# Kernel tuning notes

Hardware: AMD Instinct MI355X
Metric: run time of the kernel (lower is better)

The kernel has to match this reference:

```python
import jax, jax.numpy as jnp
import numpy as np

N_NODES = 50000
IN_CH = 128
DIM = 32
HEADS = 8
OUT_CH = 2
NEG_SLOPE = 0.2


def _glorot(key, shape):
    fan_in = shape[0]
    return jax.random.normal(key, shape, dtype=jnp.float32) / jnp.sqrt(jnp.float32(fan_in))


def gatv2_conv(x, Wl, bl, Wr, br, att, bias, src, dst, n_nodes, heads, out_c, concat):
    """PyG GATv2Conv (eval mode, add_self_loops already applied to src/dst)."""
    xl = (x @ Wl + bl).reshape(n_nodes, heads, out_c)  # [N,H,C] source transform
    xr = (x @ Wr + br).reshape(n_nodes, heads, out_c)  # [N,H,C] target transform
    # per-edge GATv2 score: a^T LeakyReLU(xl[j] + xr[i])
    e = jax.nn.leaky_relu(xl[src] + xr[dst], NEG_SLOPE)          # [E,H,C]
    score = jnp.einsum('ehc,hc->eh', e, att)                      # [E,H]
    # segment softmax over incoming edges of each target node
    smax = jax.ops.segment_max(score, dst, num_segments=n_nodes)  # [N,H]
    ex = jnp.exp(score - smax[dst])
    denom = jax.ops.segment_sum(ex, dst, num_segments=n_nodes)
    alpha = ex / (denom[dst] + 1e-16)                             # [E,H]
    out = jax.ops.segment_sum(alpha[:, :, None] * xl[src], dst, num_segments=n_nodes)  # [N,H,C]
    if concat:
        out = out.reshape(n_nodes, heads * out_c)
    else:
        out = out.mean(axis=1)
    return out + bias


def setup_inputs() -> dict:
    key = jax.random.key(0)
    ks = jax.random.split(key, 20)
    x = jax.random.normal(ks[0], (N_NODES, IN_CH), dtype=jnp.float32)
    edge_index = jax.random.randint(ks[1], (2, 400000), 0, N_NODES, dtype=jnp.int32)
    H, C = HEADS, DIM
    hid = H * C  # 256
    params = {
        'Wl1': _glorot(ks[2], (IN_CH, hid)), 'bl1': jnp.zeros((hid,), jnp.float32),
        'Wr1': _glorot(ks[3], (IN_CH, hid)), 'br1': jnp.zeros((hid,), jnp.float32),
        'att1': _glorot(ks[4], (H, C)), 'b1': jnp.zeros((hid,), jnp.float32),
        'Wl3': _glorot(ks[5], (hid, hid)), 'bl3': jnp.zeros((hid,), jnp.float32),
        'Wr3': _glorot(ks[6], (hid, hid)), 'br3': jnp.zeros((hid,), jnp.float32),
        'att3': _glorot(ks[7], (H, C)), 'b3': jnp.zeros((hid,), jnp.float32),
        'Wl2': _glorot(ks[8], (hid, OUT_CH)), 'bl2': jnp.zeros((OUT_CH,), jnp.float32),
        'Wr2': _glorot(ks[9], (hid, OUT_CH)), 'br2': jnp.zeros((OUT_CH,), jnp.float32),
        'att2': _glorot(ks[10], (1, OUT_CH)), 'b2': jnp.zeros((OUT_CH,), jnp.float32),
    }
    return {'x': x, 'edge_index': edge_index, **params}


def reference(x, edge_index, Wl1, bl1, Wr1, br1, att1, b1,
              Wl3, bl3, Wr3, br3, att3, b3,
              Wl2, bl2, Wr2, br2, att2, b2):
    n = x.shape[0]
    loop = jnp.arange(n, dtype=edge_index.dtype)
    src = jnp.concatenate([edge_index[0], loop])  # PyG add_self_loops
    dst = jnp.concatenate([edge_index[1], loop])
    # dropout layers are no-ops in eval mode
    h = jax.nn.elu(gatv2_conv(x, Wl1, bl1, Wr1, br1, att1, b1, src, dst, n, HEADS, DIM, True))
    h = jax.nn.elu(gatv2_conv(h, Wl3, bl3, Wr3, br3, att3, b3, src, dst, n, HEADS, DIM, True))
    h = gatv2_conv(h, Wl2, bl2, Wr2, br2, att2, b2, src, dst, n, 1, OUT_CH, False)
    return jax.nn.log_softmax(h, axis=-1)
```

## Files before the change

### kernel.cpp

```cpp
#include <hip/hip_runtime.h>
#include <cstdint>
#include <cstddef>


typedef __attribute__((ext_vector_type(8))) _Float16 v8h;
typedef __attribute__((ext_vector_type(2))) _Float16 h2;
typedef __attribute__((ext_vector_type(2))) __fp16 h2r;
typedef __attribute__((ext_vector_type(4))) float v4f;

__device__ __forceinline__ float lrelu(float v) { return fmaxf(v, 0.2f * v); }
__device__ __forceinline__ float elu1(float v)  { return v > 0.f ? v : expm1f(v); }

__device__ __forceinline__ unsigned short f2h(float f) {
  _Float16 h = (_Float16)f;
  return __builtin_bit_cast(unsigned short, h);
}
__device__ __forceinline__ float h2f(unsigned short s) {
  return (float)__builtin_bit_cast(_Float16, s);
}

__device__ __forceinline__ h2 cvt_pk(float a, float b) {
  h2r t = __builtin_amdgcn_cvt_pkrtz(a, b);
  return __builtin_bit_cast(h2, t);
}
__device__ __forceinline__ h2 pk2(float a) { return cvt_pk(a, a); }

__device__ __forceinline__ h2 lrelu_pk(h2 v) {
  unsigned int u = __builtin_bit_cast(unsigned int, v) & 0x7FFF7FFFu;
  h2 av = __builtin_bit_cast(h2, u);
  h2 c6 = {(_Float16)0.6f, (_Float16)0.6f};
  h2 c4 = {(_Float16)0.4f, (_Float16)0.4f};
  return v * c6 + av * c4;
}

__device__ __forceinline__ float dot2(h2 a, h2 b, float c) {
#if __has_builtin(__builtin_amdgcn_fdot2)
  return __builtin_amdgcn_fdot2(__builtin_bit_cast(h2r, a),
                                __builtin_bit_cast(h2r, b), c, false);
#else
  return fmaf((float)a[0], (float)b[0], fmaf((float)a[1], (float)b[1], c));
#endif
}

__device__ __forceinline__ void gl_lds16(const void* g, void* l) {
  __builtin_amdgcn_global_load_lds(
      (const __attribute__((address_space(1))) unsigned int*)g,
      (__attribute__((address_space(3))) unsigned int*)l, 16, 0, 0);
}


__global__ void k_count(const int* __restrict__ dst, int* __restrict__ deg, int E) {
  int e = blockIdx.x * blockDim.x + threadIdx.x;
  if (e < E) atomicAdd(&deg[dst[e]], 1);
}

__global__ __launch_bounds__(256) void k_bsum(const int* __restrict__ deg, int n,
                                              int* __restrict__ bsum) {
  __shared__ int red[256];
  int t = threadIdx.x, bid = blockIdx.x;
  int i0 = bid * 1024 + t * 4;
  int s = 0;
  if (i0 + 3 < n) {
    int4 v = *(const int4*)&deg[i0];
    s = v.x + v.y + v.z + v.w;
  } else {
#pragma unroll
    for (int j = 0; j < 4; ++j)
      if (i0 + j < n) s += deg[i0 + j];
  }
  red[t] = s;
  __syncthreads();
  for (int off = 128; off > 0; off >>= 1) {
    if (t < off) red[t] += red[t + off];
    __syncthreads();
  }
  if (t == 0) bsum[bid] = red[0];
}

__global__ __launch_bounds__(256) void k_offsets(const int* __restrict__ deg,
                                                 const int* __restrict__ bsum,
                                                 int nb, int n,
                                                 int* __restrict__ offs,
                                                 int* __restrict__ cursor) {
  __shared__ int sc[256];
  int t = threadIdx.x, bid = blockIdx.x;
  int base = 0;
  for (int b = 0; b < bid; ++b) base += bsum[b];
  int i0 = bid * 1024 + t * 4;
  int v0 = 0, v1 = 0, v2 = 0, v3 = 0;
  if (i0 + 3 < n) {
    int4 v = *(const int4*)&deg[i0];
    v0 = v.x; v1 = v.y; v2 = v.z; v3 = v.w;
  } else {
    if (i0 < n)     v0 = deg[i0];
    if (i0 + 1 < n) v1 = deg[i0 + 1];
    if (i0 + 2 < n) v2 = deg[i0 + 2];
    if (i0 + 3 < n) v3 = deg[i0 + 3];
  }
  int s = v0 + v1 + v2 + v3;
  sc[t] = s;
  __syncthreads();
  for (int off = 1; off < 256; off <<= 1) {
    int x = (t >= off) ? sc[t - off] : 0;
    __syncthreads();
    sc[t] += x;
    __syncthreads();
  }
  int run = base + sc[t] - s;
  int o0 = run, o1 = run + v0, o2 = o1 + v1, o3 = o2 + v2;
  if (i0 + 3 < n) {
    *(int4*)&offs[i0] = make_int4(o0, o1, o2, o3);
    *(int4*)&cursor[i0] = make_int4(o0, o1, o2, o3);
  } else {
    if (i0 < n)     { offs[i0] = o0;     cursor[i0] = o0; }
    if (i0 + 1 < n) { offs[i0 + 1] = o1; cursor[i0 + 1] = o1; }
    if (i0 + 2 < n) { offs[i0 + 2] = o2; cursor[i0 + 2] = o2; }
    if (i0 + 3 < n) { offs[i0 + 3] = o3; cursor[i0 + 3] = o3; }
  }
  if (bid == nb - 1 && t == 255) offs[n] = base + sc[255];
}

__global__ void k_scatter(const int* __restrict__ src, const int* __restrict__ dst,
                          int* __restrict__ cursor, int* __restrict__ csr_src, int E) {
  int e = blockIdx.x * blockDim.x + threadIdx.x;
  if (e < E) {
    int pos = atomicAdd(&cursor[dst[e]], 1);
    csr_src[pos] = src[e];
  }
}


__global__ void k_split(const float* __restrict__ Wl, const float* __restrict__ Wr,
                        int K, int logK, unsigned short* __restrict__ Bt) {
  int idx = blockIdx.x * blockDim.x + threadIdx.x;
  if (idx >= 512 * K) return;
  int n = idx >> logK;
  int k = idx & (K - 1);
  float w = (n < 256) ? Wl[(size_t)k * 256 + n] : Wr[(size_t)k * 256 + (n - 256)];
  Bt[idx] = f2h(w);
}


__global__ void k_quantA(const float* __restrict__ X, int Nreal, int total4,
                         unsigned short* __restrict__ Hh) {
  int idx = blockIdx.x * blockDim.x + threadIdx.x;
  if (idx >= total4) return;
  int row = idx >> 5;
  ushort4 uh;
  if (row < Nreal) {
    float4 v = *(const float4*)&X[(size_t)idx * 4];
    uh.x = f2h(v.x); uh.y = f2h(v.y); uh.z = f2h(v.z); uh.w = f2h(v.w);
  } else {
    uh = make_ushort4(0, 0, 0, 0);
  }
  *(ushort4*)&Hh[(size_t)idx * 4] = uh;
}


__global__ __launch_bounds__(256) void k_gemm_mfma(
    const unsigned short* __restrict__ A_g,
    int Nreal, int K,
    const unsigned short* __restrict__ Bt,
    const float* __restrict__ bl, const float* __restrict__ br,
    unsigned short* __restrict__ xl_h, unsigned short* __restrict__ xr_h) {
  __shared__ __align__(16) short Ah[2][64 * 32];
  __shared__ __align__(16) short Bh[2][256 * 32];

  const int tid = threadIdx.x;
  const int lane = tid & 63;
  const int wid = tid >> 6;
  const int l15 = lane & 15, g = lane >> 4;
  const int bm = blockIdx.x * 64;
  const int half = blockIdx.y;
  const int bn = half * 256;

  v4f acc[4][4];
#pragma unroll
  for (int m = 0; m < 4; ++m)
#pragma unroll
    for (int n = 0; n < 4; ++n) acc[m][n] = (v4f)(0.f);

  const int arow = tid >> 2, aslot = tid & 3;
  const int aoct = aslot ^ ((arow >> 1) & 3);
  const unsigned gaBase = (unsigned)(bm + arow) * K + aoct * 8;

  auto STAGE = [&](int buf, int k0) {
    gl_lds16(A_g + (gaBase + k0), &Ah[buf][wid * 512]);
#pragma unroll
    for (int it = 0; it < 4; ++it) {
      int task = it * 256 + tid;
      int col = task >> 2, slot = task & 3;
      int oct = slot ^ ((col >> 1) & 3);
      unsigned gb = (unsigned)(bn + col) * K + k0 + oct * 8;
      gl_lds16(Bt + gb, &Bh[buf][it * 2048 + wid * 512]);
    }
  };

  const int nt = K >> 5;
  STAGE(0, 0);
  for (int t = 0; t < nt; ++t) {
    const int cur = t & 1;
    if (t + 1 < nt) {
      STAGE(cur ^ 1, (t + 1) << 5);
      asm volatile("s_waitcnt vmcnt(5)" ::: "memory");
    } else {
      asm volatile("s_waitcnt vmcnt(0)" ::: "memory");
    }
    __builtin_amdgcn_sched_barrier(0);
    __builtin_amdgcn_s_barrier();

    v8h a_h[4], b_h[4];
#pragma unroll
    for (int m = 0; m < 4; ++m) {
      int r = m * 16 + l15;
      int s = g ^ ((r >> 1) & 3);
      a_h[m] = *(const v8h*)&Ah[cur][r * 32 + s * 8];
    }
#pragma unroll
    for (int n = 0; n < 4; ++n) {
      int c = wid * 64 + n * 16 + l15;
      int s = g ^ ((c >> 1) & 3);
      b_h[n] = *(const v8h*)&Bh[cur][c * 32 + s * 8];
    }
#pragma unroll
    for (int m = 0; m < 4; ++m)
#pragma unroll
      for (int n = 0; n < 4; ++n)
        acc[m][n] = __builtin_amdgcn_mfma_f32_16x16x32_f16(a_h[m], b_h[n], acc[m][n], 0, 0, 0);
    __builtin_amdgcn_s_barrier();
  }

  float* scr = (float*)&Bh[0][0] + wid * 320;
  const int erow = lane >> 2, ecq = lane & 3;
  unsigned short* outp = half ? xr_h : xl_h;
  const float* bias = half ? br : bl;
#pragma unroll
  for (int m = 0; m < 4; ++m) {
#pragma unroll
    for (int n = 0; n < 4; ++n) {
#pragma unroll
      for (int r = 0; r < 4; ++r) scr[(g * 4 + r) * 20 + l15] = acc[m][n][r];
      float4 v = *(const float4*)&scr[erow * 20 + ecq * 4];
      int row = bm + m * 16 + erow;
      if (row < Nreal) {
        int col = wid * 64 + n * 16 + ecq * 4;
        float4 bv = *(const float4*)&bias[col];
        ushort4 u;
        u.x = f2h(v.x + bv.x); u.y = f2h(v.y + bv.y);
        u.z = f2h(v.z + bv.z); u.w = f2h(v.w + bv.w);
        *(ushort4*)&outp[(size_t)row * 256 + col] = u;
      }
    }
  }
}


__global__ __launch_bounds__(256) void k_edge(
    const unsigned short* __restrict__ xl_h,
    const unsigned short* __restrict__ xr_h,
    const int* __restrict__ offs, const int* __restrict__ csr_src,
    const float* __restrict__ att,
    const float* __restrict__ bias,
    unsigned short* __restrict__ hout,
    int n) {
  int lane = threadIdx.x & 63;
  int node = blockIdx.x * (blockDim.x >> 6) + (threadIdx.x >> 6);
  if (node >= n) return;

  const unsigned lb = (unsigned)(lane << 2);
  float4 attf = *(const float4*)&att[lb];
  h2 atta = cvt_pk(attf.x, attf.y);
  h2 attb = cvt_pk(attf.z, attf.w);
  const unsigned noff = ((unsigned)node << 8) + lb;
  uint2 urx = *(const uint2*)(xr_h + noff);
  h2 xra = __builtin_bit_cast(h2, urx.x), xrb = __builtin_bit_cast(h2, urx.y);

  uint2 us = *(const uint2*)(xl_h + noff);
  h2 acca = __builtin_bit_cast(h2, us.x), accb = __builtin_bit_cast(h2, us.y);
  float p = dot2(lrelu_pk(acca + xra), atta, 0.f);
  p = dot2(lrelu_pk(accb + xrb), attb, p);
  p += __shfl_xor(p, 1);
  p += __shfl_xor(p, 2);
  p += __shfl_xor(p, 4);
  float m = p, d = 1.f;

  int e0 = offs[node], e1 = offs[node + 1];
  int e = e0;
  for (; e + 1 < e1; e += 2) {
    int j1 = csr_src[e], j2 = csr_src[e + 1];
    uint2 u1 = *(const uint2*)(xl_h + (((unsigned)j1 << 8) + lb));
    uint2 u2 = *(const uint2*)(xl_h + (((unsigned)j2 << 8) + lb));
    h2 x1a = __builtin_bit_cast(h2, u1.x), x1b = __builtin_bit_cast(h2, u1.y);
    h2 x2a = __builtin_bit_cast(h2, u2.x), x2b = __builtin_bit_cast(h2, u2.y);
    float p1 = dot2(lrelu_pk(x1a + xra), atta, 0.f);
    p1 = dot2(lrelu_pk(x1b + xrb), attb, p1);
    float p2 = dot2(lrelu_pk(x2a + xra), atta, 0.f);
    p2 = dot2(lrelu_pk(x2b + xrb), attb, p2);
    p1 += __shfl_xor(p1, 1); p2 += __shfl_xor(p2, 1);
    p1 += __shfl_xor(p1, 2); p2 += __shfl_xor(p2, 2);
    p1 += __shfl_xor(p1, 4); p2 += __shfl_xor(p2, 4);
    float m12 = fmaxf(p1, p2);
    float w1 = __expf(p1 - m12), w2 = __expf(p2 - m12);
    float d12 = w1 + w2;
    h2 w1p = pk2(w1), w2p = pk2(w2);
    h2 ca = x1a * w1p + x2a * w2p;
    h2 cb = x1b * w1p + x2b * w2p;
    float mN = fmaxf(m, m12);
    float r  = __expf(m - mN);
    float r2 = __expf(m12 - mN);
    d = fmaf(d, r, d12 * r2);
    h2 rp = pk2(r), r2p = pk2(r2);
    acca = acca * rp + ca * r2p;
    accb = accb * rp + cb * r2p;
    m = mN;
  }
  if (e < e1) {
    int j = csr_src[e];
    uint2 u = *(const uint2*)(xl_h + (((unsigned)j << 8) + lb));
    h2 xa = __builtin_bit_cast(h2, u.x), xb = __builtin_bit_cast(h2, u.y);
    float p1 = dot2(lrelu_pk(xa + xra), atta, 0.f);
    p1 = dot2(lrelu_pk(xb + xrb), attb, p1);
    p1 += __shfl_xor(p1, 1);
    p1 += __shfl_xor(p1, 2);
    p1 += __shfl_xor(p1, 4);
    float mN = fmaxf(m, p1);
    float r = __expf(m - mN), w1 = __expf(p1 - mN);
    d = fmaf(d, r, w1);
    h2 rp = pk2(r), w1p = pk2(w1);
    acca = acca * rp + xa * w1p;
    accb = accb * rp + xb * w1p;
  }

  float inv = 1.f / (d + 1e-16f);
  float4 b4 = *(const float4*)&bias[lb];
  float o0 = elu1(fmaf((float)acca[0], inv, b4.x));
  float o1 = elu1(fmaf((float)acca[1], inv, b4.y));
  float o2 = elu1(fmaf((float)accb[0], inv, b4.z));
  float o3 = elu1(fmaf((float)accb[1], inv, b4.w));
  ushort4 uo;
  uo.x = f2h(o0); uo.y = f2h(o1); uo.z = f2h(o2); uo.w = f2h(o3);
  *(ushort4*)(hout + noff) = uo;
}


__global__ __launch_bounds__(256) void k_lin3(
    const unsigned short* __restrict__ hq,
    const float* __restrict__ Wl, const float* __restrict__ bl,
    const float* __restrict__ Wr, const float* __restrict__ br,
    float* __restrict__ xlr3,
    int n) {
  int lane = threadIdx.x & 63;
  int node = blockIdx.x * (blockDim.x >> 6) + (threadIdx.x >> 6);
  if (node >= n) return;
  ushort4 uh = *(const ushort4*)(hq + (((unsigned)node << 8) + (lane << 2)));
  float hv[4] = {h2f(uh.x), h2f(uh.y), h2f(uh.z), h2f(uh.w)};
  float al0 = 0.f, al1 = 0.f, ar0 = 0.f, ar1 = 0.f;
#pragma unroll
  for (int j = 0; j < 4; ++j) {
    int k = lane * 4 + j;
    al0 = fmaf(hv[j], Wl[k * 2 + 0], al0);
    al1 = fmaf(hv[j], Wl[k * 2 + 1], al1);
    ar0 = fmaf(hv[j], Wr[k * 2 + 0], ar0);
    ar1 = fmaf(hv[j], Wr[k * 2 + 1], ar1);
  }
#pragma unroll
  for (int s = 1; s < 64; s <<= 1) {
    al0 += __shfl_xor(al0, s);
    al1 += __shfl_xor(al1, s);
    ar0 += __shfl_xor(ar0, s);
    ar1 += __shfl_xor(ar1, s);
  }
  if (lane == 0) {
    float4 o = make_float4(al0 + bl[0], al1 + bl[1], ar0 + br[0], ar1 + br[1]);
    *(float4*)&xlr3[(size_t)node * 4] = o;
  }
}


__global__ void k_edge3(const float* __restrict__ xlr3,
                        const int* __restrict__ offs, const int* __restrict__ csr_src,
                        const float* __restrict__ att,
                        const float* __restrict__ b,
                        float* __restrict__ out, int n) {
  int i = blockIdx.x * blockDim.x + threadIdx.x;
  if (i >= n) return;
  float a0 = att[0], a1 = att[1];
  float xr0 = xlr3[(size_t)i * 4 + 2], xr1 = xlr3[(size_t)i * 4 + 3];
  float sl0 = xlr3[(size_t)i * 4 + 0], sl1 = xlr3[(size_t)i * 4 + 1];
  float m = lrelu(sl0 + xr0) * a0 + lrelu(sl1 + xr1) * a1;
  float d = 1.f, ac0 = sl0, ac1 = sl1;
  int e0 = offs[i], e1 = offs[i + 1];
  for (int e = e0; e < e1; ++e) {
    int j = csr_src[e];
    float xl0 = xlr3[(size_t)j * 4 + 0], xl1 = xlr3[(size_t)j * 4 + 1];
    float p = lrelu(xl0 + xr0) * a0 + lrelu(xl1 + xr1) * a1;
    float mN = fmaxf(m, p);
    float r = __expf(m - mN), w = __expf(p - mN);
    d = fmaf(d, r, w);
    ac0 = fmaf(ac0, r, w * xl0);
    ac1 = fmaf(ac1, r, w * xl1);
    m = mN;
  }
  float inv = 1.f / (d + 1e-16f);
  float o0 = fmaf(ac0, inv, b[0]);
  float o1 = fmaf(ac1, inv, b[1]);
  float mx = fmaxf(o0, o1);
  float lse = mx + logf(expf(o0 - mx) + expf(o1 - mx));
  out[(size_t)i * 2 + 0] = o0 - lse;
  out[(size_t)i * 2 + 1] = o1 - lse;
}


static inline size_t align_up(size_t v, size_t a) { return (v + a - 1) & ~(a - 1); }

extern "C" void kernel_launch(void* const* d_in, const int* in_sizes, int n_in,
                              void* d_out, int out_size, void* d_ws, size_t ws_size,
                              hipStream_t stream) {
  const float* x    = (const float*)d_in[0];
  const int*   ei   = (const int*)d_in[1];
  const float* Wl1  = (const float*)d_in[2];
  const float* bl1  = (const float*)d_in[3];
  const float* Wr1  = (const float*)d_in[4];
  const float* br1  = (const float*)d_in[5];
  const float* att1 = (const float*)d_in[6];
  const float* b1   = (const float*)d_in[7];
  const float* Wl3  = (const float*)d_in[8];
  const float* bl3  = (const float*)d_in[9];
  const float* Wr3  = (const float*)d_in[10];
  const float* br3  = (const float*)d_in[11];
  const float* att3 = (const float*)d_in[12];
  const float* b3   = (const float*)d_in[13];
  const float* Wl2  = (const float*)d_in[14];
  const float* bl2  = (const float*)d_in[15];
  const float* Wr2  = (const float*)d_in[16];
  const float* br2  = (const float*)d_in[17];
  const float* att2 = (const float*)d_in[18];
  const float* b2   = (const float*)d_in[19];

  const int N = in_sizes[0] / 128;
  const int E = in_sizes[1] / 2;
  const int Npad = ((N + 63) / 64) * 64;
  const int* srcp = ei;
  const int* dstp = ei + E;

  char* w = (char*)d_ws;
  size_t off = 0;
  int* deg     = (int*)(w + off); off = align_up(off + (size_t)N * 4, 256);
  int* offs    = (int*)(w + off); off = align_up(off + (size_t)(N + 1) * 4, 256);
  int* cursor  = (int*)(w + off); off = align_up(off + (size_t)N * 4, 256);
  int* csr_src = (int*)(w + off); off = align_up(off + (size_t)E * 4, 256);
  int* bsum    = (int*)(w + off); off = align_up(off + (size_t)256 * 4, 256);
  unsigned short* x_h  = (unsigned short*)(w + off); off = align_up(off + (size_t)Npad * 128 * 2, 256);
  unsigned short* h_h  = (unsigned short*)(w + off); off = align_up(off + (size_t)Npad * 256 * 2, 256);
  unsigned short* xlh  = (unsigned short*)(w + off); off = align_up(off + (size_t)N * 256 * 2, 256);
  unsigned short* xrh  = (unsigned short*)(w + off); off = align_up(off + (size_t)N * 256 * 2, 256);
  float* xlr3  = (float*)(w + off); off = align_up(off + (size_t)N * 4 * 4, 256);
  unsigned short* Bt1 = (unsigned short*)(w + off); off = align_up(off + (size_t)512 * 128 * 2, 256);
  unsigned short* Bt2 = (unsigned short*)(w + off); off = align_up(off + (size_t)512 * 256 * 2, 256);
  (void)ws_size;

  const int nb = (N + 1023) / 1024;

  hipMemsetAsync(deg, 0, (size_t)N * 4, stream);
  k_count<<<(E + 255) / 256, 256, 0, stream>>>(dstp, deg, E);
  k_bsum<<<nb, 256, 0, stream>>>(deg, N, bsum);
  k_offsets<<<nb, 256, 0, stream>>>(deg, bsum, nb, N, offs, cursor);
  k_scatter<<<(E + 255) / 256, 256, 0, stream>>>(srcp, dstp, cursor, csr_src, E);

  k_split<<<(512 * 128 + 255) / 256, 256, 0, stream>>>(Wl1, Wr1, 128, 7, Bt1);
  k_split<<<(512 * 256 + 255) / 256, 256, 0, stream>>>(Wl3, Wr3, 256, 8, Bt2);
  {
    int total4 = Npad * 128 / 4;
    k_quantA<<<(total4 + 255) / 256, 256, 0, stream>>>(x, N, total4, x_h);
  }
  hipMemsetAsync(h_h + (size_t)N * 256, 0, (size_t)(Npad - N) * 256 * 2, stream);

  dim3 ggrid(Npad / 64, 2);
  int nodeBlocks = (N + 3) / 4;

  k_gemm_mfma<<<ggrid, 256, 0, stream>>>(x_h, N, 128, Bt1, bl1, br1, xlh, xrh);
  k_edge<<<nodeBlocks, 256, 0, stream>>>(xlh, xrh, offs, csr_src, att1, b1, h_h, N);

  k_gemm_mfma<<<ggrid, 256, 0, stream>>>(h_h, N, 256, Bt2, bl3, br3, xlh, xrh);
  k_edge<<<nodeBlocks, 256, 0, stream>>>(xlh, xrh, offs, csr_src, att3, b3, h_h, N);

  k_lin3<<<nodeBlocks, 256, 0, stream>>>(h_h, Wl2, bl2, Wr2, br2, xlr3, N);
  k_edge3<<<(N + 255) / 256, 256, 0, stream>>>(xlr3, offs, csr_src, att2, b2,
                                               (float*)d_out, N);
}
```

Measured before the change: 240.6 us.

## Process each node with 32 lanes and 16-byte gathers in GATv2 edge kernel

The edge aggregation kernel now assigns 32 lanes per target node instead of 64. Each lane handles 8 fp16 channels through 16-byte loads, so a block covers 8 nodes. Each head's score reduction becomes a 4-lane sum done with DPP quad permutes rather than three shuffle-xor steps. This is meant to cut the number of load instructions and the cross-lane reduction overhead per gathered edge row, at the cost of more registers per lane. The launch grids are adjusted so the per-node block count for k_lin3 stays unchanged.

```diff
diff --git a/kernel.cpp b/kernel.cpp
--- a/kernel.cpp
+++ b/kernel.cpp
@@ -40,6 +40,14 @@
 #else
   return fmaf((float)a[0], (float)b[0], fmaf((float)a[1], (float)b[1], c));
 #endif
+}
+
+__device__ __forceinline__ float quad_sum(float p) {
+  int t1 = __builtin_amdgcn_update_dpp(0, __float_as_int(p), 0xB1, 0xF, 0xF, true);
+  p += __int_as_float(t1);
+  int t2 = __builtin_amdgcn_update_dpp(0, __float_as_int(p), 0x4E, 0xF, 0xF, true);
+  p += __int_as_float(t2);
+  return p;
 }
 
 __device__ __forceinline__ void gl_lds16(const void* g, void* l) {
@@ -263,83 +271,97 @@
     const float* __restrict__ bias,
     unsigned short* __restrict__ hout,
     int n) {
-  int lane = threadIdx.x & 63;
-  int node = blockIdx.x * (blockDim.x >> 6) + (threadIdx.x >> 6);
+  int lane = threadIdx.x & 31;
+  int node = blockIdx.x * (blockDim.x >> 5) + (threadIdx.x >> 5);
   if (node >= n) return;
 
-  const unsigned lb = (unsigned)(lane << 2);
-  float4 attf = *(const float4*)&att[lb];
-  h2 atta = cvt_pk(attf.x, attf.y);
-  h2 attb = cvt_pk(attf.z, attf.w);
-  const unsigned noff = ((unsigned)node << 8) + lb;
-  uint2 urx = *(const uint2*)(xr_h + noff);
-  h2 xra = __builtin_bit_cast(h2, urx.x), xrb = __builtin_bit_cast(h2, urx.y);
-
-  uint2 us = *(const uint2*)(xl_h + noff);
-  h2 acca = __builtin_bit_cast(h2, us.x), accb = __builtin_bit_cast(h2, us.y);
-  float p = dot2(lrelu_pk(acca + xra), atta, 0.f);
-  p = dot2(lrelu_pk(accb + xrb), attb, p);
-  p += __shfl_xor(p, 1);
-  p += __shfl_xor(p, 2);
-  p += __shfl_xor(p, 4);
-  float m = p, d = 1.f;
+  const unsigned cb = ((unsigned)(lane >> 2) << 5) + ((unsigned)(lane & 3) << 3);
+  float4 af0 = *(const float4*)&att[cb];
+  float4 af1 = *(const float4*)&att[cb + 4];
+  h2 att0 = cvt_pk(af0.x, af0.y), att1 = cvt_pk(af0.z, af0.w);
+  h2 att2 = cvt_pk(af1.x, af1.y), att3 = cvt_pk(af1.z, af1.w);
+  const unsigned noff = ((unsigned)node << 8) + cb;
+  uint4 urx = *(const uint4*)(xr_h + noff);
+  h2 xr0 = __builtin_bit_cast(h2, urx.x), xr1 = __builtin_bit_cast(h2, urx.y);
+  h2 xr2 = __builtin_bit_cast(h2, urx.z), xr3 = __builtin_bit_cast(h2, urx.w);
+  const unsigned short* xlb = xl_h + cb;
+
+  auto score = [&](h2 a, h2 b, h2 c, h2 dd) -> float {
+    float p = dot2(lrelu_pk(a + xr0), att0, 0.f);
+    p = dot2(lrelu_pk(b + xr1), att1, p);
+    p = dot2(lrelu_pk(c + xr2), att2, p);
+    p = dot2(lrelu_pk(dd + xr3), att3, p);
+    return quad_sum(p);
+  };
+
+  uint4 us = *(const uint4*)(xl_h + noff);
+  h2 a0 = __builtin_bit_cast(h2, us.x), a1 = __builtin_bit_cast(h2, us.y);
+  h2 a2 = __builtin_bit_cast(h2, us.z), a3 = __builtin_bit_cast(h2, us.w);
+  float m = score(a0, a1, a2, a3), d = 1.f;
 
   int e0 = offs[node], e1 = offs[node + 1];
   int e = e0;
   for (; e + 1 < e1; e += 2) {
     int j1 = csr_src[e], j2 = csr_src[e + 1];
-    uint2 u1 = *(const uint2*)(xl_h + (((unsigned)j1 << 8) + lb));
-    uint2 u2 = *(const uint2*)(xl_h + (((unsigned)j2 << 8) + lb));
-    h2 x1a = __builtin_bit_cast(h2, u1.x), x1b = __builtin_bit_cast(h2, u1.y);
-    h2 x2a = __builtin_bit_cast(h2, u2.x), x2b = __builtin_bit_cast(h2, u2.y);
-    float p1 = dot2(lrelu_pk(x1a + xra), atta, 0.f);
-    p1 = dot2(lrelu_pk(x1b + xrb), attb, p1);
-    float p2 = dot2(lrelu_pk(x2a + xra), atta, 0.f);
-    p2 = dot2(lrelu_pk(x2b + xrb), attb, p2);
-    p1 += __shfl_xor(p1, 1); p2 += __shfl_xor(p2, 1);
-    p1 += __shfl_xor(p1, 2); p2 += __shfl_xor(p2, 2);
-    p1 += __shfl_xor(p1, 4); p2 += __shfl_xor(p2, 4);
+    uint4 u1 = *(const uint4*)(xlb + ((unsigned)j1 << 8));
+    uint4 u2 = *(const uint4*)(xlb + ((unsigned)j2 << 8));
+    h2 x10 = __builtin_bit_cast(h2, u1.x), x11 = __builtin_bit_cast(h2, u1.y);
+    h2 x12 = __builtin_bit_cast(h2, u1.z), x13 = __builtin_bit_cast(h2, u1.w);
+    h2 x20 = __builtin_bit_cast(h2, u2.x), x21 = __builtin_bit_cast(h2, u2.y);
+    h2 x22 = __builtin_bit_cast(h2, u2.z), x23 = __builtin_bit_cast(h2, u2.w);
+    float p1 = score(x10, x11, x12, x13);
+    float p2 = score(x20, x21, x22, x23);
     float m12 = fmaxf(p1, p2);
     float w1 = __expf(p1 - m12), w2 = __expf(p2 - m12);
     float d12 = w1 + w2;
     h2 w1p = pk2(w1), w2p = pk2(w2);
-    h2 ca = x1a * w1p + x2a * w2p;
-    h2 cb = x1b * w1p + x2b * w2p;
+    h2 c0 = x10 * w1p + x20 * w2p;
+    h2 c1 = x11 * w1p + x21 * w2p;
+    h2 c2 = x12 * w1p + x22 * w2p;
+    h2 c3 = x13 * w1p + x23 * w2p;
     float mN = fmaxf(m, m12);
-    float r  = __expf(m - mN);
-    float r2 = __expf(m12 - mN);
+    float r = __expf(m - mN), r2 = __expf(m12 - mN);
     d = fmaf(d, r, d12 * r2);
     h2 rp = pk2(r), r2p = pk2(r2);
-    acca = acca * rp + ca * r2p;
-    accb = accb * rp + cb * r2p;
+    a0 = a0 * rp + c0 * r2p;
+    a1 = a1 * rp + c1 * r2p;
+    a2 = a2 * rp + c2 * r2p;
+    a3 = a3 * rp + c3 * r2p;
     m = mN;
   }
   if (e < e1) {
     int j = csr_src[e];
-    uint2 u = *(const uint2*)(xl_h + (((unsigned)j << 8) + lb));
-    h2 xa = __builtin_bit_cast(h2, u.x), xb = __builtin_bit_cast(h2, u.y);
-    float p1 = dot2(lrelu_pk(xa + xra), atta, 0.f);
-    p1 = dot2(lrelu_pk(xb + xrb), attb, p1);
-    p1 += __shfl_xor(p1, 1);
-    p1 += __shfl_xor(p1, 2);
-    p1 += __shfl_xor(p1, 4);
+    uint4 u = *(const uint4*)(xlb + ((unsigned)j << 8));
+    h2 x0 = __builtin_bit_cast(h2, u.x), x1 = __builtin_bit_cast(h2, u.y);
+    h2 x2 = __builtin_bit_cast(h2, u.z), x3 = __builtin_bit_cast(h2, u.w);
+    float p1 = score(x0, x1, x2, x3);
     float mN = fmaxf(m, p1);
     float r = __expf(m - mN), w1 = __expf(p1 - mN);
     d = fmaf(d, r, w1);
     h2 rp = pk2(r), w1p = pk2(w1);
-    acca = acca * rp + xa * w1p;
-    accb = accb * rp + xb * w1p;
+    a0 = a0 * rp + x0 * w1p;
+    a1 = a1 * rp + x1 * w1p;
+    a2 = a2 * rp + x2 * w1p;
+    a3 = a3 * rp + x3 * w1p;
   }
 
   float inv = 1.f / (d + 1e-16f);
-  float4 b4 = *(const float4*)&bias[lb];
-  float o0 = elu1(fmaf((float)acca[0], inv, b4.x));
-  float o1 = elu1(fmaf((float)acca[1], inv, b4.y));
-  float o2 = elu1(fmaf((float)accb[0], inv, b4.z));
-  float o3 = elu1(fmaf((float)accb[1], inv, b4.w));
-  ushort4 uo;
-  uo.x = f2h(o0); uo.y = f2h(o1); uo.z = f2h(o2); uo.w = f2h(o3);
-  *(ushort4*)(hout + noff) = uo;
+  float4 b0 = *(const float4*)&bias[cb];
+  float4 b1 = *(const float4*)&bias[cb + 4];
+  float o0 = elu1(fmaf((float)a0[0], inv, b0.x));
+  float o1 = elu1(fmaf((float)a0[1], inv, b0.y));
+  float o2 = elu1(fmaf((float)a1[0], inv, b0.z));
+  float o3 = elu1(fmaf((float)a1[1], inv, b0.w));
+  float o4 = elu1(fmaf((float)a2[0], inv, b1.x));
+  float o5 = elu1(fmaf((float)a2[1], inv, b1.y));
+  float o6 = elu1(fmaf((float)a3[0], inv, b1.z));
+  float o7 = elu1(fmaf((float)a3[1], inv, b1.w));
+  uint4 uo;
+  uo.x = (unsigned)f2h(o0) | ((unsigned)f2h(o1) << 16);
+  uo.y = (unsigned)f2h(o2) | ((unsigned)f2h(o3) << 16);
+  uo.z = (unsigned)f2h(o4) | ((unsigned)f2h(o5) << 16);
+  uo.w = (unsigned)f2h(o6) | ((unsigned)f2h(o7) << 16);
+  *(uint4*)(hout + noff) = uo;
 }
 
 
@@ -476,7 +498,7 @@
   hipMemsetAsync(h_h + (size_t)N * 256, 0, (size_t)(Npad - N) * 256 * 2, stream);
 
   dim3 ggrid(Npad / 64, 2);
-  int nodeBlocks = (N + 3) / 4;
+  int nodeBlocks = (N + 7) / 8;
 
   k_gemm_mfma<<<ggrid, 256, 0, stream>>>(x_h, N, 128, Bt1, bl1, br1, xlh, xrh);
   k_edge<<<nodeBlocks, 256, 0, stream>>>(xlh, xrh, offs, csr_src, att1, b1, h_h, N);
@@ -484,7 +506,7 @@
   k_gemm_mfma<<<ggrid, 256, 0, stream>>>(h_h, N, 256, Bt2, bl3, br3, xlh, xrh);
   k_edge<<<nodeBlocks, 256, 0, stream>>>(xlh, xrh, offs, csr_src, att3, b3, h_h, N);
 
-  k_lin3<<<nodeBlocks, 256, 0, stream>>>(h_h, Wl2, bl2, Wr2, br2, xlr3, N);
+  k_lin3<<<nodeBlocks * 2, 256, 0, stream>>>(h_h, Wl2, bl2, Wr2, br2, xlr3, N);
   k_edge3<<<(N + 255) / 256, 256, 0, stream>>>(xlr3, offs, csr_src, att2, b2,
                                                (float*)d_out, N);
 }
```

Result: faster. 229.7 us (-4.5%).
